# Kernel tuning notes

Measured on AMD Instinct MI355X. Metric: run time of the kernel, lower is better.

The kernel has to match this reference:

```python
import math
import jax, jax.numpy as jnp
import numpy as np

B, D, C = 1024, 512, 100000
S = 30.0
M = 0.3
COS_M = math.cos(M)
SIN_M = math.sin(M)
TH = math.cos(math.pi - M)
MM = math.sin(math.pi - M) * M
EPS = 1e-12  # torch F.normalize eps


def _l2norm(x):
    n = jnp.sqrt(jnp.sum(x * x, axis=-1, keepdims=True))
    return x / jnp.maximum(n, EPS)


def setup_inputs() -> dict:
    key = jax.random.key(0)
    k1, k2, k3 = jax.random.split(key, 3)
    features = jax.random.normal(k1, (B, D), dtype=jnp.float32)
    # xavier_uniform_ for weight [C, D]
    limit = math.sqrt(6.0 / (C + D))
    weight = jax.random.uniform(k2, (C, D), dtype=jnp.float32, minval=-limit, maxval=limit)
    targets = jax.random.randint(k3, (B,), 0, C, dtype=jnp.int64)
    return {"features": features, "weight": weight, "targets": targets}


def reference(features, weight, targets):
    # cosine similarity via normalized GEMM: [B, C]
    cosine = _l2norm(features) @ _l2norm(weight).T
    cosine = cosine.astype(jnp.float32)
    sine = jnp.sqrt(jnp.maximum(1.0 - cosine * cosine, 0.0))
    phi = cosine * COS_M - sine * SIN_M
    # easy_margin=False branch
    phi = jnp.where(cosine > TH, phi, cosine - MM)
    # one-hot blend (ls_eps == 0): target column gets phi, rest keep cosine
    one_hot = targets[:, None] == jnp.arange(C)[None, :]
    logits = jnp.where(one_hot, phi, cosine) * S
    # CrossEntropyLoss (mean reduction)
    logp = jax.nn.log_softmax(logits, axis=-1)
    loss = -jnp.mean(jnp.take_along_axis(logp, targets[:, None], axis=1))
    return loss
```

## Files before the change

### kernel.cpp

```cpp
#include <hip/hip_runtime.h>

#define B_ROWS 1024
#define D_DIM  512
#define C_CLS  100000
#define N_TILES 782
#define GRID_NJ 98

typedef unsigned short u16;
typedef __attribute__((ext_vector_type(8))) short bf16x8;
typedef __attribute__((ext_vector_type(4))) float f32x4;

__device__ __forceinline__ u16 f2bf(float f) {
  unsigned u = __float_as_uint(f);
  u += 0x7fffu + ((u >> 16) & 1u);
  return (u16)(u >> 16);
}

__device__ __forceinline__ bf16x8 pack8(float4 a, float4 b) {
  union { bf16x8 v; unsigned u[4]; } r;
  r.u[0] = __builtin_amdgcn_perm(__float_as_uint(a.y), __float_as_uint(a.x), 0x07060302u);
  r.u[1] = __builtin_amdgcn_perm(__float_as_uint(a.w), __float_as_uint(a.z), 0x07060302u);
  r.u[2] = __builtin_amdgcn_perm(__float_as_uint(b.y), __float_as_uint(b.x), 0x07060302u);
  r.u[3] = __builtin_amdgcn_perm(__float_as_uint(b.w), __float_as_uint(b.z), 0x07060302u);
  return r.v;
}

__device__ __forceinline__ void gll16(const void* g, void* l) {
  __builtin_amdgcn_global_load_lds(
      (const __attribute__((address_space(1))) unsigned int*)g,
      (__attribute__((address_space(3))) unsigned int*)l, 16, 0, 0);
}

__global__ void prep_kernel(const float* __restrict__ feat,
                            const float* __restrict__ wt,
                            u16* __restrict__ fn, u16* __restrict__ wb,
                            float* __restrict__ psum)
{
  const int row  = blockIdx.x * 4 + (threadIdx.x >> 6);
  const int lane = threadIdx.x & 63;
  const float* src = (row < B_ROWS) ? feat + (size_t)row * D_DIM
                                    : wt + (size_t)(row - B_ROWS) * D_DIM;
  u16* dst = (row < B_ROWS) ? fn + (size_t)row * D_DIM
                            : wb + (size_t)(row - B_ROWS) * D_DIM;
  const float4* r = (const float4*)src;
  float4 v0 = r[lane];
  float4 v1 = r[lane + 64];
  float ss = v0.x*v0.x + v0.y*v0.y + v0.z*v0.z + v0.w*v0.w
           + v1.x*v1.x + v1.y*v1.y + v1.z*v1.z + v1.w*v1.w;
#pragma unroll
  for (int m = 1; m < 64; m <<= 1) ss += __shfl_xor(ss, m);
  const float inv = 1.0f / fmaxf(sqrtf(ss), 1e-12f);
  ushort4 o0, o1;
  o0.x = f2bf(v0.x * inv); o0.y = f2bf(v0.y * inv);
  o0.z = f2bf(v0.z * inv); o0.w = f2bf(v0.w * inv);
  o1.x = f2bf(v1.x * inv); o1.y = f2bf(v1.y * inv);
  o1.z = f2bf(v1.z * inv); o1.w = f2bf(v1.w * inv);
  ushort4* od = (ushort4*)dst;
  od[lane]      = o0;
  od[lane + 64] = o1;
  if (row < B_ROWS && lane == 0) psum[row] = 0.0f;
}

__global__ __launch_bounds__(256, 4) void arc_gemm_pre(
    const u16* __restrict__ fn, const u16* __restrict__ wb,
    const int* __restrict__ targets, float* __restrict__ psum,
    float* __restrict__ tlogit)
{
  __shared__ u16 As[128 * 32];
  __shared__ u16 Ws[128 * 32];
  __shared__ int tg[128];

  const int tid = threadIdx.x;
  const int bx  = blockIdx.x;
  const int xcd = bx & 7;
  const int l   = bx >> 3;
  const int tile_ni = (l >> 3) * 8 + xcd;
  if (tile_ni >= N_TILES) return;
  const int tile_m = (l & 7) << 7;
  const int tile_n = tile_ni << 7;

  if (tid < 128) tg[tid] = targets[tile_m + tid];

  const int wave = tid >> 6, lane = tid & 63;
  const int wm = wave >> 1, wno = wave & 1;
  const int quad = lane >> 4, l15 = lane & 15;

  f32x4 acc[4][4] = {};

  const int srow   = tid >> 2;
  const int schunk = (tid & 3) ^ ((tid >> 3) & 3);
  const u16* Ag = fn + (size_t)(tile_m + srow) * D_DIM + schunk * 8;
  const int wr0 = tile_n + srow;
  const int wr1 = wr0 + 64;
  const u16* Wg0 = wb + (size_t)min(wr0, C_CLS - 1) * D_DIM + schunk * 8;
  const u16* Wg1 = wb + (size_t)min(wr1, C_CLS - 1) * D_DIM + schunk * 8;
  u16* Asd0 = As + tid * 8;
  u16* Asd1 = As + 2048 + tid * 8;
  u16* Wsd0 = Ws + tid * 8;
  u16* Wsd1 = Ws + 2048 + tid * 8;

  const int rsw = (quad ^ ((l15 >> 1) & 3)) * 8;
  const u16* ApA = As + (wm * 64 + l15) * 32 + rsw;
  const u16* ApW = Ws + (wno * 64 + l15) * 32 + rsw;

  for (int k0 = 0; k0 < D_DIM; k0 += 32) {
    gll16(Ag + k0, Asd0);
    gll16(Ag + 64 * D_DIM + k0, Asd1);
    gll16(Wg0 + k0, Wsd0);
    gll16(Wg1 + k0, Wsd1);
    __syncthreads();
    bf16x8 af[4], wf[4];
#pragma unroll
    for (int r = 0; r < 4; r++) af[r] = *(const bf16x8*)(ApA + r * 16 * 32);
#pragma unroll
    for (int r = 0; r < 4; r++) wf[r] = *(const bf16x8*)(ApW + r * 16 * 32);
#pragma unroll
    for (int rm = 0; rm < 4; rm++)
#pragma unroll
      for (int rn = 0; rn < 4; rn++)
        acc[rm][rn] = __builtin_amdgcn_mfma_f32_16x16x32_bf16(
            af[rm], wf[rn], acc[rm][rn], 0, 0, 0);
    __syncthreads();
  }

  const float Sc   = 30.0f;
  const float COSM = 0.9553364891256060f;
  const float SINM = 0.2955202066613396f;
  const float THc  = -0.9553364891256060f;
  const float MMc  = 0.0886560619984019f;

#pragma unroll
  for (int rm = 0; rm < 4; rm++) {
#pragma unroll
    for (int reg = 0; reg < 4; reg++) {
      const int bl = wm * 64 + rm * 16 + quad * 4 + reg;
      const int b = tile_m + bl;
      const int tgt = tg[bl];
      float s = 0.0f;
#pragma unroll
      for (int rn = 0; rn < 4; rn++) {
        const int c = tile_n + wno * 64 + rn * 16 + l15;
        const float cosv = acc[rm][rn][reg];
        float logit = Sc * cosv;
        if (c == tgt) {
          const float sine = sqrtf(fmaxf(1.0f - cosv * cosv, 0.0f));
          float phi = cosv * COSM - sine * SINM;
          phi = (cosv > THc) ? phi : (cosv - MMc);
          logit = Sc * phi;
          tlogit[b] = logit;
        }
        s += (c < C_CLS) ? __expf(logit - 30.0f) : 0.0f;
      }
      s += __shfl_xor(s, 1);
      s += __shfl_xor(s, 2);
      s += __shfl_xor(s, 4);
      s += __shfl_xor(s, 8);
      if (l15 == 0) atomicAdd(psum + b, s);
    }
  }
}

__global__ void norm_feat_kernel(const float* __restrict__ in,
                                 u16* __restrict__ out,
                                 float* __restrict__ psum)
{
  const int row  = blockIdx.x * 4 + (threadIdx.x >> 6);
  const int lane = threadIdx.x & 63;
  const float4* r = (const float4*)(in + (size_t)row * D_DIM);
  float4 v0 = r[lane];
  float4 v1 = r[lane + 64];
  float ss = v0.x*v0.x + v0.y*v0.y + v0.z*v0.z + v0.w*v0.w
           + v1.x*v1.x + v1.y*v1.y + v1.z*v1.z + v1.w*v1.w;
#pragma unroll
  for (int m = 1; m < 64; m <<= 1) ss += __shfl_xor(ss, m);
  const float inv = 1.0f / fmaxf(sqrtf(ss), 1e-12f);
  ushort4 o0, o1;
  o0.x = f2bf(v0.x * inv); o0.y = f2bf(v0.y * inv);
  o0.z = f2bf(v0.z * inv); o0.w = f2bf(v0.w * inv);
  o1.x = f2bf(v1.x * inv); o1.y = f2bf(v1.y * inv);
  o1.z = f2bf(v1.z * inv); o1.w = f2bf(v1.w * inv);
  ushort4* orow = (ushort4*)(out + (size_t)row * D_DIM);
  orow[lane]      = o0;
  orow[lane + 64] = o1;
  if (lane == 0) psum[row] = 0.0f;
}

__global__ __launch_bounds__(256, 4) void arc_gemm_raw(
    const u16* __restrict__ fn, const float* __restrict__ wt,
    const int* __restrict__ targets, float* __restrict__ psum,
    float* __restrict__ tlogit)
{
  __shared__ u16 As[128 * 32];
  __shared__ u16 Ws[128 * 32];
  __shared__ int tg[128];
  __shared__ float winv[128];

  const int tid = threadIdx.x;
  const int bx  = blockIdx.x;
  const int xcd = bx & 7;
  const int l   = bx >> 3;
  const int tile_ni = (l >> 3) * 8 + xcd;
  if (tile_ni >= N_TILES) return;
  const int tile_m = (l & 7) << 7;
  const int tile_n = tile_ni << 7;

  if (tid < 128) tg[tid] = targets[tile_m + tid];

  const int wave = tid >> 6, lane = tid & 63;
  const int wm = wave >> 1, wno = wave & 1;
  const int quad = lane >> 4, l15 = lane & 15;

  f32x4 acc[4][4] = {};

  const int srow   = tid >> 2;
  const int schunk = (tid & 3) ^ ((tid >> 3) & 3);
  const u16* Ag = fn + (size_t)(tile_m + srow) * D_DIM + schunk * 8;
  u16* Asd0 = As + tid * 8;
  u16* Asd1 = As + 2048 + tid * 8;
  const int wr0 = tile_n + srow;
  const int wr1 = wr0 + 64;
  const float* Wg0 = wt + (size_t)min(wr0, C_CLS - 1) * D_DIM + schunk * 8;
  const float* Wg1 = wt + (size_t)min(wr1, C_CLS - 1) * D_DIM + schunk * 8;
  u16* Wsd0 = Ws + tid * 8;
  u16* Wsd1 = Ws + 2048 + tid * 8;

  const int rsw = (quad ^ ((l15 >> 1) & 3)) * 8;
  const u16* ApA = As + (wm * 64 + l15) * 32 + rsw;
  const u16* ApW = Ws + (wno * 64 + l15) * 32 + rsw;

  float ssq0 = 0.0f, ssq1 = 0.0f;

  for (int k0 = 0; k0 < D_DIM; k0 += 32) {
    const float4 wa = *(const float4*)(Wg0 + k0);
    const float4 wb2 = *(const float4*)(Wg0 + k0 + 4);
    const float4 wc = *(const float4*)(Wg1 + k0);
    const float4 wd = *(const float4*)(Wg1 + k0 + 4);
    gll16(Ag + k0, Asd0);
    gll16(Ag + 64 * D_DIM + k0, Asd1);
    ssq0 += wa.x*wa.x + wa.y*wa.y + wa.z*wa.z + wa.w*wa.w
          + wb2.x*wb2.x + wb2.y*wb2.y + wb2.z*wb2.z + wb2.w*wb2.w;
    ssq1 += wc.x*wc.x + wc.y*wc.y + wc.z*wc.z + wc.w*wc.w
          + wd.x*wd.x + wd.y*wd.y + wd.z*wd.z + wd.w*wd.w;
    *(bf16x8*)Wsd0 = pack8(wa, wb2);
    *(bf16x8*)Wsd1 = pack8(wc, wd);
    __syncthreads();
    bf16x8 af[4], wf[4];
#pragma unroll
    for (int r = 0; r < 4; r++) af[r] = *(const bf16x8*)(ApA + r * 16 * 32);
#pragma unroll
    for (int r = 0; r < 4; r++) wf[r] = *(const bf16x8*)(ApW + r * 16 * 32);
#pragma unroll
    for (int rm = 0; rm < 4; rm++)
#pragma unroll
      for (int rn = 0; rn < 4; rn++)
        acc[rm][rn] = __builtin_amdgcn_mfma_f32_16x16x32_bf16(
            af[rm], wf[rn], acc[rm][rn], 0, 0, 0);
    __syncthreads();
  }

  ssq0 += __shfl_xor(ssq0, 1); ssq0 += __shfl_xor(ssq0, 2);
  ssq1 += __shfl_xor(ssq1, 1); ssq1 += __shfl_xor(ssq1, 2);
  if ((tid & 3) == 0) {
    winv[srow]      = 1.0f / fmaxf(sqrtf(ssq0), 1e-12f);
    winv[srow + 64] = 1.0f / fmaxf(sqrtf(ssq1), 1e-12f);
  }
  __syncthreads();

  float wiv[4];
#pragma unroll
  for (int rn = 0; rn < 4; rn++) wiv[rn] = winv[wno * 64 + rn * 16 + l15];

  const float Sc   = 30.0f;
  const float COSM = 0.9553364891256060f;
  const float SINM = 0.2955202066613396f;
  const float THc  = -0.9553364891256060f;
  const float MMc  = 0.0886560619984019f;

#pragma unroll
  for (int rm = 0; rm < 4; rm++) {
#pragma unroll
    for (int reg = 0; reg < 4; reg++) {
      const int bl = wm * 64 + rm * 16 + quad * 4 + reg;
      const int b = tile_m + bl;
      const int tgt = tg[bl];
      float s = 0.0f;
#pragma unroll
      for (int rn = 0; rn < 4; rn++) {
        const int c = tile_n + wno * 64 + rn * 16 + l15;
        const float cosv = acc[rm][rn][reg] * wiv[rn];
        float logit = Sc * cosv;
        if (c == tgt) {
          const float sine = sqrtf(fmaxf(1.0f - cosv * cosv, 0.0f));
          float phi = cosv * COSM - sine * SINM;
          phi = (cosv > THc) ? phi : (cosv - MMc);
          logit = Sc * phi;
          tlogit[b] = logit;
        }
        s += (c < C_CLS) ? __expf(logit - 30.0f) : 0.0f;
      }
      s += __shfl_xor(s, 1);
      s += __shfl_xor(s, 2);
      s += __shfl_xor(s, 4);
      s += __shfl_xor(s, 8);
      if (l15 == 0) atomicAdd(psum + b, s);
    }
  }
}

__global__ void finalize_loss(const float* __restrict__ psum,
                              const float* __restrict__ tlogit,
                              float* __restrict__ out)
{
  const int tid = threadIdx.x;
  float s = 0.0f;
  for (int i = tid; i < B_ROWS; i += 256)
    s += 30.0f + logf(psum[i]) - tlogit[i];
#pragma unroll
  for (int m = 1; m < 64; m <<= 1) s += __shfl_xor(s, m);
  __shared__ float red[4];
  if ((tid & 63) == 0) red[tid >> 6] = s;
  __syncthreads();
  if (tid == 0) out[0] = (red[0] + red[1] + red[2] + red[3]) * (1.0f / B_ROWS);
}

extern "C" void kernel_launch(void* const* d_in, const int* in_sizes, int n_in,
                              void* d_out, int out_size, void* d_ws, size_t ws_size,
                              hipStream_t stream) {
  const float* feat = (const float*)d_in[0];
  const float* wt   = (const float*)d_in[1];
  const int*   tgt  = (const int*)d_in[2];
  float* out = (float*)d_out;
  char* ws = (char*)d_ws;

  const size_t fn_bytes = (size_t)B_ROWS * D_DIM * 2;
  const size_t wb_bytes = (size_t)C_CLS * D_DIM * 2;
  const size_t tail     = 2 * (size_t)B_ROWS * sizeof(float);

  if (ws_size >= fn_bytes + wb_bytes + tail) {
    u16* fn = (u16*)ws;
    u16* wb = (u16*)(ws + fn_bytes);
    float* psum = (float*)(ws + fn_bytes + wb_bytes);
    float* tlogit = psum + B_ROWS;
    prep_kernel<<<(B_ROWS + C_CLS) / 4, 256, 0, stream>>>(feat, wt, fn, wb, psum);
    arc_gemm_pre<<<GRID_NJ * 8 * 8, 256, 0, stream>>>(fn, wb, tgt, psum, tlogit);
    finalize_loss<<<1, 256, 0, stream>>>(psum, tlogit, out);
  } else {
    u16* fn = (u16*)ws;
    float* psum = (float*)(ws + fn_bytes);
    float* tlogit = psum + B_ROWS;
    norm_feat_kernel<<<B_ROWS / 4, 256, 0, stream>>>(feat, fn, psum);
    arc_gemm_raw<<<GRID_NJ * 8 * 8, 256, 0, stream>>>(fn, wt, tgt, psum, tlogit);
    finalize_loss<<<1, 256, 0, stream>>>(psum, tlogit, out);
  }
}
```

Measured before the change: 480.6 us.

## Double K-step per barrier, grid-stride prep, and block-level psum reduction

The GEMM main loop now stages a 64-wide K slice per iteration, using larger LDS tiles with an 8-way XOR swizzle, and runs two MFMA sub-steps per pair of barriers. This halves the number of synchronizations and global-to-LDS issue rounds. The prep kernel becomes a grid-stride loop over a fixed 2048-block grid instead of one wave per row. Per-row exp-sums are combined across the two column waves in shared memory before a single atomic per row. The cost is doubled LDS use per block, which may reduce occupancy.

Measured after the change: 425.3 us. 11.5% less time.

```diff
diff --git a/kernel.cpp b/kernel.cpp
--- a/kernel.cpp
+++ b/kernel.cpp
@@ -31,34 +31,36 @@
       (__attribute__((address_space(3))) unsigned int*)l, 16, 0, 0);
 }
 
-__global__ void prep_kernel(const float* __restrict__ feat,
-                            const float* __restrict__ wt,
-                            u16* __restrict__ fn, u16* __restrict__ wb,
-                            float* __restrict__ psum)
-{
-  const int row  = blockIdx.x * 4 + (threadIdx.x >> 6);
+__global__ __launch_bounds__(256) void prep_kernel(
+    const float* __restrict__ feat, const float* __restrict__ wt,
+    u16* __restrict__ fn, u16* __restrict__ wb, float* __restrict__ psum)
+{
   const int lane = threadIdx.x & 63;
-  const float* src = (row < B_ROWS) ? feat + (size_t)row * D_DIM
-                                    : wt + (size_t)(row - B_ROWS) * D_DIM;
-  u16* dst = (row < B_ROWS) ? fn + (size_t)row * D_DIM
-                            : wb + (size_t)(row - B_ROWS) * D_DIM;
-  const float4* r = (const float4*)src;
-  float4 v0 = r[lane];
-  float4 v1 = r[lane + 64];
-  float ss = v0.x*v0.x + v0.y*v0.y + v0.z*v0.z + v0.w*v0.w
-           + v1.x*v1.x + v1.y*v1.y + v1.z*v1.z + v1.w*v1.w;
-#pragma unroll
-  for (int m = 1; m < 64; m <<= 1) ss += __shfl_xor(ss, m);
-  const float inv = 1.0f / fmaxf(sqrtf(ss), 1e-12f);
-  ushort4 o0, o1;
-  o0.x = f2bf(v0.x * inv); o0.y = f2bf(v0.y * inv);
-  o0.z = f2bf(v0.z * inv); o0.w = f2bf(v0.w * inv);
-  o1.x = f2bf(v1.x * inv); o1.y = f2bf(v1.y * inv);
-  o1.z = f2bf(v1.z * inv); o1.w = f2bf(v1.w * inv);
-  ushort4* od = (ushort4*)dst;
-  od[lane]      = o0;
-  od[lane + 64] = o1;
-  if (row < B_ROWS && lane == 0) psum[row] = 0.0f;
+  const int wid  = blockIdx.x * 4 + (threadIdx.x >> 6);
+  const int nw   = gridDim.x * 4;
+  for (int row = wid; row < B_ROWS + C_CLS; row += nw) {
+    const float* src = (row < B_ROWS) ? feat + (size_t)row * D_DIM
+                                      : wt + (size_t)(row - B_ROWS) * D_DIM;
+    u16* dst = (row < B_ROWS) ? fn + (size_t)row * D_DIM
+                              : wb + (size_t)(row - B_ROWS) * D_DIM;
+    const float4* r = (const float4*)src;
+    float4 v0 = r[lane];
+    float4 v1 = r[lane + 64];
+    float ss = v0.x*v0.x + v0.y*v0.y + v0.z*v0.z + v0.w*v0.w
+             + v1.x*v1.x + v1.y*v1.y + v1.z*v1.z + v1.w*v1.w;
+#pragma unroll
+    for (int m = 1; m < 64; m <<= 1) ss += __shfl_xor(ss, m);
+    const float inv = 1.0f / fmaxf(sqrtf(ss), 1e-12f);
+    ushort4 o0, o1;
+    o0.x = f2bf(v0.x * inv); o0.y = f2bf(v0.y * inv);
+    o0.z = f2bf(v0.z * inv); o0.w = f2bf(v0.w * inv);
+    o1.x = f2bf(v1.x * inv); o1.y = f2bf(v1.y * inv);
+    o1.z = f2bf(v1.z * inv); o1.w = f2bf(v1.w * inv);
+    ushort4* od = (ushort4*)dst;
+    od[lane]      = o0;
+    od[lane + 64] = o1;
+    if (row < B_ROWS && lane == 0) psum[row] = 0.0f;
+  }
 }
 
 __global__ __launch_bounds__(256, 4) void arc_gemm_pre(
@@ -66,9 +68,10 @@
     const int* __restrict__ targets, float* __restrict__ psum,
     float* __restrict__ tlogit)
 {
-  __shared__ u16 As[128 * 32];
-  __shared__ u16 Ws[128 * 32];
+  __shared__ u16 As[128 * 64];
+  __shared__ u16 Ws[128 * 64];
   __shared__ int tg[128];
+  __shared__ float pr[256];
 
   const int tid = threadIdx.x;
   const int bx  = blockIdx.x;
@@ -87,39 +90,58 @@
 
   f32x4 acc[4][4] = {};
 
-  const int srow   = tid >> 2;
-  const int schunk = (tid & 3) ^ ((tid >> 3) & 3);
-  const u16* Ag = fn + (size_t)(tile_m + srow) * D_DIM + schunk * 8;
-  const int wr0 = tile_n + srow;
-  const int wr1 = wr0 + 64;
-  const u16* Wg0 = wb + (size_t)min(wr0, C_CLS - 1) * D_DIM + schunk * 8;
-  const u16* Wg1 = wb + (size_t)min(wr1, C_CLS - 1) * D_DIM + schunk * 8;
-  u16* Asd0 = As + tid * 8;
-  u16* Asd1 = As + 2048 + tid * 8;
-  u16* Wsd0 = Ws + tid * 8;
-  u16* Wsd1 = Ws + 2048 + tid * 8;
-
-  const int rsw = (quad ^ ((l15 >> 1) & 3)) * 8;
-  const u16* ApA = As + (wm * 64 + l15) * 32 + rsw;
-  const u16* ApW = Ws + (wno * 64 + l15) * 32 + rsw;
-
-  for (int k0 = 0; k0 < D_DIM; k0 += 32) {
-    gll16(Ag + k0, Asd0);
-    gll16(Ag + 64 * D_DIM + k0, Asd1);
-    gll16(Wg0 + k0, Wsd0);
-    gll16(Wg1 + k0, Wsd1);
+  const int srow8  = tid >> 3;
+  const int schunk = (tid & 7) ^ (srow8 & 7);
+  const u16* Abase = fn + (size_t)(tile_m + srow8) * D_DIM + schunk * 8;
+  unsigned woff[4];
+#pragma unroll
+  for (int i = 0; i < 4; i++) {
+    const int wrow = tile_n + i * 32 + srow8;
+    woff[i] = (unsigned)min(wrow, C_CLS - 1) * D_DIM;
+  }
+  const u16* Wchunk = wb + schunk * 8;
+  u16* Asd = As + tid * 8;
+  u16* Wsd = Ws + tid * 8;
+
+  const u16* ApA = As + (wm * 64 + l15) * 64;
+  const u16* ApW = Ws + (wno * 64 + l15) * 64;
+  const int sw0 = ((quad    ) ^ (l15 & 7)) * 8;
+  const int sw1 = ((quad ^ 4) ^ (l15 & 7)) * 8;
+
+  for (int k0 = 0; k0 < D_DIM; k0 += 64) {
+#pragma unroll
+    for (int i = 0; i < 4; i++) {
+      gll16(Abase + k0 + i * 32 * D_DIM, Asd + i * 2048);
+      gll16(Wchunk + woff[i] + k0,       Wsd + i * 2048);
+    }
     __syncthreads();
-    bf16x8 af[4], wf[4];
-#pragma unroll
-    for (int r = 0; r < 4; r++) af[r] = *(const bf16x8*)(ApA + r * 16 * 32);
-#pragma unroll
-    for (int r = 0; r < 4; r++) wf[r] = *(const bf16x8*)(ApW + r * 16 * 32);
-#pragma unroll
-    for (int rm = 0; rm < 4; rm++)
-#pragma unroll
-      for (int rn = 0; rn < 4; rn++)
-        acc[rm][rn] = __builtin_amdgcn_mfma_f32_16x16x32_bf16(
-            af[rm], wf[rn], acc[rm][rn], 0, 0, 0);
+    {
+      bf16x8 af[4], wf[4];
+#pragma unroll
+      for (int r = 0; r < 4; r++) af[r] = *(const bf16x8*)(ApA + r * 1024 + sw0);
+#pragma unroll
+      for (int r = 0; r < 4; r++) wf[r] = *(const bf16x8*)(ApW + r * 1024 + sw0);
+#pragma unroll
+      for (int rm = 0; rm < 4; rm++)
+#pragma unroll
+        for (int rn = 0; rn < 4; rn++)
+          acc[rm][rn] = __builtin_amdgcn_mfma_f32_16x16x32_bf16(
+              af[rm], wf[rn], acc[rm][rn], 0, 0, 0);
+    }
+    __builtin_amdgcn_sched_barrier(0);
+    {
+      bf16x8 af[4], wf[4];
+#pragma unroll
+      for (int r = 0; r < 4; r++) af[r] = *(const bf16x8*)(ApA + r * 1024 + sw1);
+#pragma unroll
+      for (int r = 0; r < 4; r++) wf[r] = *(const bf16x8*)(ApW + r * 1024 + sw1);
+#pragma unroll
+      for (int rm = 0; rm < 4; rm++)
+#pragma unroll
+        for (int rn = 0; rn < 4; rn++)
+          acc[rm][rn] = __builtin_amdgcn_mfma_f32_16x16x32_bf16(
+              af[rm], wf[rn], acc[rm][rn], 0, 0, 0);
+    }
     __syncthreads();
   }
 
@@ -155,9 +177,11 @@
       s += __shfl_xor(s, 2);
       s += __shfl_xor(s, 4);
       s += __shfl_xor(s, 8);
-      if (l15 == 0) atomicAdd(psum + b, s);
-    }
-  }
+      if (l15 == 0) pr[wno * 128 + bl] = s;
+    }
+  }
+  __syncthreads();
+  if (tid < 128) atomicAdd(psum + tile_m + tid, pr[tid] + pr[128 + tid]);
 }
 
 __global__ void norm_feat_kernel(const float* __restrict__ in,
@@ -341,7 +365,7 @@
     u16* wb = (u16*)(ws + fn_bytes);
     float* psum = (float*)(ws + fn_bytes + wb_bytes);
     float* tlogit = psum + B_ROWS;
-    prep_kernel<<<(B_ROWS + C_CLS) / 4, 256, 0, stream>>>(feat, wt, fn, wb, psum);
+    prep_kernel<<<2048, 256, 0, stream>>>(feat, wt, fn, wb, psum);
     arc_gemm_pre<<<GRID_NJ * 8 * 8, 256, 0, stream>>>(fn, wb, tgt, psum, tlogit);
     finalize_loss<<<1, 256, 0, stream>>>(psum, tlogit, out);
   } else {
```

## Double-buffer GEMM LDS tiles, batch psum atomics, grid-stride prep kernel

Applied to the files above, without the earlier changes.

Splits the GEMM's LDS A/W tiles into two buffers so the next k-slice's global-to-LDS load is issued before computing the current one, which halves the barriers per iteration and overlaps memory with MFMA work. Per-row partial sums from the two column waves are combined in shared memory before a single atomicAdd per row, cutting global atomics in half. The prep kernel becomes a persistent grid-stride loop over 2048 blocks, with each wave processing two rows at once for more memory-level parallelism. The cost is double the LDS use, which may limit occupancy under the 4-blocks-per-CU launch bound.

New measurement: 440.9 us. -8.3%, faster.

```diff
diff --git a/kernel.cpp b/kernel.cpp
--- a/kernel.cpp
+++ b/kernel.cpp
@@ -31,34 +31,61 @@
       (__attribute__((address_space(3))) unsigned int*)l, 16, 0, 0);
 }
 
-__global__ void prep_kernel(const float* __restrict__ feat,
-                            const float* __restrict__ wt,
-                            u16* __restrict__ fn, u16* __restrict__ wb,
-                            float* __restrict__ psum)
-{
-  const int row  = blockIdx.x * 4 + (threadIdx.x >> 6);
-  const int lane = threadIdx.x & 63;
-  const float* src = (row < B_ROWS) ? feat + (size_t)row * D_DIM
-                                    : wt + (size_t)(row - B_ROWS) * D_DIM;
-  u16* dst = (row < B_ROWS) ? fn + (size_t)row * D_DIM
-                            : wb + (size_t)(row - B_ROWS) * D_DIM;
-  const float4* r = (const float4*)src;
-  float4 v0 = r[lane];
-  float4 v1 = r[lane + 64];
-  float ss = v0.x*v0.x + v0.y*v0.y + v0.z*v0.z + v0.w*v0.w
-           + v1.x*v1.x + v1.y*v1.y + v1.z*v1.z + v1.w*v1.w;
-#pragma unroll
-  for (int m = 1; m < 64; m <<= 1) ss += __shfl_xor(ss, m);
-  const float inv = 1.0f / fmaxf(sqrtf(ss), 1e-12f);
-  ushort4 o0, o1;
-  o0.x = f2bf(v0.x * inv); o0.y = f2bf(v0.y * inv);
-  o0.z = f2bf(v0.z * inv); o0.w = f2bf(v0.w * inv);
-  o1.x = f2bf(v1.x * inv); o1.y = f2bf(v1.y * inv);
-  o1.z = f2bf(v1.z * inv); o1.w = f2bf(v1.w * inv);
-  ushort4* od = (ushort4*)dst;
-  od[lane]      = o0;
-  od[lane + 64] = o1;
-  if (row < B_ROWS && lane == 0) psum[row] = 0.0f;
+__global__ __launch_bounds__(256) void prep_kernel(
+    const float* __restrict__ feat, const float* __restrict__ wt,
+    u16* __restrict__ fn, u16* __restrict__ wb, float* __restrict__ psum)
+{
+  const int lane  = threadIdx.x & 63;
+  const int wid   = blockIdx.x * 4 + (threadIdx.x >> 6);
+  const int nw    = gridDim.x * 4;
+  const int total = B_ROWS + C_CLS;
+  for (int row = wid; row < total; row += 2 * nw) {
+    const int rowb  = row + nw;
+    const bool hasb = rowb < total;
+    const float* sa = (row < B_ROWS) ? feat + (size_t)row * D_DIM
+                                     : wt + (size_t)(row - B_ROWS) * D_DIM;
+    u16* da = (row < B_ROWS) ? fn + (size_t)row * D_DIM
+                             : wb + (size_t)(row - B_ROWS) * D_DIM;
+    const float* sb = sa;
+    u16* db = da;
+    if (hasb) {
+      sb = (rowb < B_ROWS) ? feat + (size_t)rowb * D_DIM
+                           : wt + (size_t)(rowb - B_ROWS) * D_DIM;
+      db = (rowb < B_ROWS) ? fn + (size_t)rowb * D_DIM
+                           : wb + (size_t)(rowb - B_ROWS) * D_DIM;
+    }
+    const float4 a0 = ((const float4*)sa)[lane];
+    const float4 a1 = ((const float4*)sa)[lane + 64];
+    const float4 b0 = ((const float4*)sb)[lane];
+    const float4 b1 = ((const float4*)sb)[lane + 64];
+    float ssa = a0.x*a0.x + a0.y*a0.y + a0.z*a0.z + a0.w*a0.w
+              + a1.x*a1.x + a1.y*a1.y + a1.z*a1.z + a1.w*a1.w;
+    float ssb = b0.x*b0.x + b0.y*b0.y + b0.z*b0.z + b0.w*b0.w
+              + b1.x*b1.x + b1.y*b1.y + b1.z*b1.z + b1.w*b1.w;
+#pragma unroll
+    for (int m = 1; m < 64; m <<= 1) {
+      ssa += __shfl_xor(ssa, m);
+      ssb += __shfl_xor(ssb, m);
+    }
+    const float inva = 1.0f / fmaxf(sqrtf(ssa), 1e-12f);
+    const float invb = 1.0f / fmaxf(sqrtf(ssb), 1e-12f);
+    ushort4 oa0, oa1, ob0, ob1;
+    oa0.x = f2bf(a0.x * inva); oa0.y = f2bf(a0.y * inva);
+    oa0.z = f2bf(a0.z * inva); oa0.w = f2bf(a0.w * inva);
+    oa1.x = f2bf(a1.x * inva); oa1.y = f2bf(a1.y * inva);
+    oa1.z = f2bf(a1.z * inva); oa1.w = f2bf(a1.w * inva);
+    ((ushort4*)da)[lane]      = oa0;
+    ((ushort4*)da)[lane + 64] = oa1;
+    if (hasb) {
+      ob0.x = f2bf(b0.x * invb); ob0.y = f2bf(b0.y * invb);
+      ob0.z = f2bf(b0.z * invb); ob0.w = f2bf(b0.w * invb);
+      ob1.x = f2bf(b1.x * invb); ob1.y = f2bf(b1.y * invb);
+      ob1.z = f2bf(b1.z * invb); ob1.w = f2bf(b1.w * invb);
+      ((ushort4*)db)[lane]      = ob0;
+      ((ushort4*)db)[lane + 64] = ob1;
+    }
+    if (row < B_ROWS && lane == 0) psum[row] = 0.0f;
+  }
 }
 
 __global__ __launch_bounds__(256, 4) void arc_gemm_pre(
@@ -66,9 +93,10 @@
     const int* __restrict__ targets, float* __restrict__ psum,
     float* __restrict__ tlogit)
 {
-  __shared__ u16 As[128 * 32];
-  __shared__ u16 Ws[128 * 32];
+  __shared__ u16 As[2][128 * 32];
+  __shared__ u16 Ws[2][128 * 32];
   __shared__ int tg[128];
+  __shared__ float pr[256];
 
   const int tid = threadIdx.x;
   const int bx  = blockIdx.x;
@@ -89,39 +117,49 @@
 
   const int srow   = tid >> 2;
   const int schunk = (tid & 3) ^ ((tid >> 3) & 3);
-  const u16* Ag = fn + (size_t)(tile_m + srow) * D_DIM + schunk * 8;
+  const u16* Ag  = fn + (size_t)(tile_m + srow) * D_DIM + schunk * 8;
+  const u16* Ag2 = Ag + 64 * D_DIM;
   const int wr0 = tile_n + srow;
   const int wr1 = wr0 + 64;
   const u16* Wg0 = wb + (size_t)min(wr0, C_CLS - 1) * D_DIM + schunk * 8;
   const u16* Wg1 = wb + (size_t)min(wr1, C_CLS - 1) * D_DIM + schunk * 8;
-  u16* Asd0 = As + tid * 8;
-  u16* Asd1 = As + 2048 + tid * 8;
-  u16* Wsd0 = Ws + tid * 8;
-  u16* Wsd1 = Ws + 2048 + tid * 8;
 
   const int rsw = (quad ^ ((l15 >> 1) & 3)) * 8;
-  const u16* ApA = As + (wm * 64 + l15) * 32 + rsw;
-  const u16* ApW = Ws + (wno * 64 + l15) * 32 + rsw;
-
-  for (int k0 = 0; k0 < D_DIM; k0 += 32) {
-    gll16(Ag + k0, Asd0);
-    gll16(Ag + 64 * D_DIM + k0, Asd1);
-    gll16(Wg0 + k0, Wsd0);
-    gll16(Wg1 + k0, Wsd1);
-    __syncthreads();
+  const u16* ApA = &As[0][(wm * 64 + l15) * 32 + rsw];
+  const u16* ApW = &Ws[0][(wno * 64 + l15) * 32 + rsw];
+
+  auto stage = [&](int b, int k0) {
+    gll16(Ag  + k0, &As[b][tid * 8]);
+    gll16(Ag2 + k0, &As[b][2048 + tid * 8]);
+    gll16(Wg0 + k0, &Ws[b][tid * 8]);
+    gll16(Wg1 + k0, &Ws[b][2048 + tid * 8]);
+  };
+  auto compute = [&](int b) {
+    const u16* pA = ApA + b * 4096;
+    const u16* pW = ApW + b * 4096;
     bf16x8 af[4], wf[4];
 #pragma unroll
-    for (int r = 0; r < 4; r++) af[r] = *(const bf16x8*)(ApA + r * 16 * 32);
-#pragma unroll
-    for (int r = 0; r < 4; r++) wf[r] = *(const bf16x8*)(ApW + r * 16 * 32);
+    for (int r = 0; r < 4; r++) af[r] = *(const bf16x8*)(pA + r * 512);
+#pragma unroll
+    for (int r = 0; r < 4; r++) wf[r] = *(const bf16x8*)(pW + r * 512);
 #pragma unroll
     for (int rm = 0; rm < 4; rm++)
 #pragma unroll
       for (int rn = 0; rn < 4; rn++)
         acc[rm][rn] = __builtin_amdgcn_mfma_f32_16x16x32_bf16(
             af[rm], wf[rn], acc[rm][rn], 0, 0, 0);
+  };
+
+  stage(0, 0);
+  __syncthreads();
+  int cur = 0;
+  for (int k0 = 32; k0 < D_DIM; k0 += 32) {
+    stage(cur ^ 1, k0);
+    compute(cur);
     __syncthreads();
-  }
+    cur ^= 1;
+  }
+  compute(cur);
 
   const float Sc   = 30.0f;
   const float COSM = 0.9553364891256060f;
@@ -155,9 +193,11 @@
       s += __shfl_xor(s, 2);
       s += __shfl_xor(s, 4);
       s += __shfl_xor(s, 8);
-      if (l15 == 0) atomicAdd(psum + b, s);
-    }
-  }
+      if (l15 == 0) pr[wno * 128 + bl] = s;
+    }
+  }
+  __syncthreads();
+  if (tid < 128) atomicAdd(psum + tile_m + tid, pr[tid] + pr[128 + tid]);
 }
 
 __global__ void norm_feat_kernel(const float* __restrict__ in,
@@ -341,7 +381,7 @@
     u16* wb = (u16*)(ws + fn_bytes);
     float* psum = (float*)(ws + fn_bytes + wb_bytes);
     float* tlogit = psum + B_ROWS;
-    prep_kernel<<<(B_ROWS + C_CLS) / 4, 256, 0, stream>>>(feat, wt, fn, wb, psum);
+    prep_kernel<<<2048, 256, 0, stream>>>(feat, wt, fn, wb, psum);
     arc_gemm_pre<<<GRID_NJ * 8 * 8, 256, 0, stream>>>(fn, wb, tgt, psum, tlogit);
     finalize_loss<<<1, 256, 0, stream>>>(psum, tlogit, out);
   } else {
```
